# Kernel tuning notes

Measured on AMD Instinct MI355X. Metric: run time of the kernel, lower is better.

The kernel has to match this reference:

```python
import jax, jax.numpy as jnp
import numpy as np

N = 4096      # number of nodes (len(batch_node))
K = 8         # number of adjacency channels
C = 256       # in_channels == out_channels
E = 131072    # number of edges (avg degree 32)


def setup_inputs() -> dict:
    key = jax.random.key(0)
    k1, k2, k3 = jax.random.split(key, 3)
    h = jax.random.normal(k1, (C, N), dtype=jnp.float32)
    X = jax.random.normal(k2, (E, K), dtype=jnp.float32)
    # sample unique (src, dst) pairs so the scatter-set has no duplicate writes
    rng = np.random.default_rng(0)
    flat = rng.choice(N * N, size=E, replace=False)
    edge_index = jnp.asarray(np.stack([flat // N, flat % N]).astype(np.int32))
    batch_node = jnp.zeros((N,), dtype=jnp.float32)
    # glorot uniform: stdv = sqrt(6 / (in + out))
    stdv = np.sqrt(6.0 / (C + C)).astype(np.float32)
    weight = jax.random.uniform(k3, (K, C, C), dtype=jnp.float32,
                                minval=-stdv, maxval=stdv)
    bias = jnp.zeros((C,), dtype=jnp.float32)
    return {"h": h, "X": X, "edge_index": edge_index,
            "batch_node": batch_node, "weight": weight, "bias": bias}


def reference(h, X, edge_index, batch_node, weight, bias):
    Kk = weight.shape[0]
    Nn = batch_node.shape[0]
    # scatter edge features into K dense [N, N] adjacency tensors
    resx = jnp.zeros((Kk, Nn, Nn), dtype=h.dtype)
    resx = resx.at[:, edge_index[0], edge_index[1]].set(X.T)
    # res[k] = h @ resx[k] : [K, C, N]
    res = jnp.einsum('cn,knm->kcm', h, resx)
    # sum_k weight[k] @ res[k] : [C, N]  (in_channels == out_channels)
    out = jnp.einsum('kio,kon->in', weight, res)
    # (res.T + bias).T == res + bias[:, None]
    return out + bias[:, None]
```

## Files before the change

### kernel.cpp

```cpp
#include <hip/hip_runtime.h>

constexpr int NN = 4096;
constexpr int KC = 8;
constexpr int CC = 256;
constexpr int NE = 131072;
constexpr int KK = KC * CC;
constexpr int CAP = 96;

typedef short bf16x8 __attribute__((ext_vector_type(8)));
typedef float f32x4 __attribute__((ext_vector_type(4)));

__device__ inline unsigned short f2bf(float f) {
    union { float f; unsigned int u; } v; v.f = f;
    unsigned int u = v.u;
    u += 0x7fffu + ((u >> 16) & 1u);
    return (unsigned short)(u >> 16);
}
__device__ inline float bf2f(unsigned short u) {
    union { unsigned int i; float f; } w; w.i = ((unsigned int)u) << 16; return w.f;
}

__global__ __launch_bounds__(256) void k_mega(
    const float* __restrict__ h, const float* __restrict__ w,
    const int* __restrict__ edge_src, const int* __restrict__ edge_dst,
    unsigned short* __restrict__ ht, unsigned short* __restrict__ A,
    int* __restrict__ cursor, int2* __restrict__ bins) {
    __shared__ float tile[32][33];
    int b = blockIdx.x;
    int t = threadIdx.x;
    if (b < 512) {
        int e = b * 256 + t;
        int d = edge_dst[e];
        int slot = atomicAdd(&cursor[d], 1);
        if (slot < CAP) bins[d * CAP + slot] = make_int2(e, edge_src[e]);
    } else if (b < 1536) {
        int tt = b - 512;
        int n0 = (tt >> 3) * 32, c0 = (tt & 7) * 32;
        int tx = t & 31, ty = t >> 5;
#pragma unroll
        for (int j = 0; j < 32; j += 8)
            tile[ty + j][tx] = h[(size_t)(c0 + ty + j) * NN + n0 + tx];
        __syncthreads();
#pragma unroll
        for (int j = 0; j < 32; j += 8)
            ht[(size_t)(n0 + ty + j) * CC + c0 + tx] = f2bf(tile[tx][ty + j]);
    } else {
        int g = (b - 1536) * 256 + t;
        int idx = g * 4;
        int o = idx & 255, k = (idx >> 8) & 7, i = idx >> 11;
        float4 wv = *reinterpret_cast<const float4*>(w + ((k << 16) | (i << 8) | o));
        ushort4 av;
        av.x = f2bf(wv.x); av.y = f2bf(wv.y); av.z = f2bf(wv.z); av.w = f2bf(wv.w);
        *reinterpret_cast<ushort4*>(A + idx) = av;
    }
}

__device__ inline void agg_accum(f32x4 acc[KC], float4 v, float4 xa, float4 xb) {
    f32x4 vv = {v.x, v.y, v.z, v.w};
    acc[0] += xa.x * vv; acc[1] += xa.y * vv;
    acc[2] += xa.z * vv; acc[3] += xa.w * vv;
    acc[4] += xb.x * vv; acc[5] += xb.y * vv;
    acc[6] += xb.z * vv; acc[7] += xb.w * vv;
}

__global__ __launch_bounds__(256) void k_agg(
    const int* __restrict__ cursor, const int2* __restrict__ bins,
    const float* __restrict__ X, const unsigned short* __restrict__ ht,
    unsigned short* __restrict__ agg) {
    __shared__ f32x4 part[2][KC][64];
    const int wid  = __builtin_amdgcn_readfirstlane(threadIdx.x >> 6);
    const int lane = threadIdx.x & 63;
    const int m    = wid >> 1;
    const int half = wid & 1;
    const int n = blockIdx.x * 2 + m;
    int cnt = cursor[n];
    cnt = cnt > CAP ? CAP : cnt;
    const int h0 = (cnt + 1) >> 1;
    const int ps = n * CAP + (half ? h0 : 0);
    const int pe = n * CAP + (half ? cnt : h0);
    const float4* X4 = reinterpret_cast<const float4*>(X);

    f32x4 acc[KC] = {};

    int p = ps;
    for (; p + 8 <= pe; p += 8) {
        int2 q[8];
        ushort4 u[8];
#pragma unroll
        for (int j = 0; j < 8; ++j) q[j] = bins[p + j];
#pragma unroll
        for (int j = 0; j < 8; ++j)
            u[j] = *(const ushort4*)(ht + (size_t)q[j].y * CC + 4 * lane);
#pragma unroll
        for (int j = 0; j < 8; ++j) {
            float4 v = {bf2f(u[j].x), bf2f(u[j].y), bf2f(u[j].z), bf2f(u[j].w)};
            agg_accum(acc, v, X4[q[j].x * 2], X4[q[j].x * 2 + 1]);
        }
    }
    for (; p < pe; ++p) {
        int2 q = bins[p];
        ushort4 u = *(const ushort4*)(ht + (size_t)q.y * CC + 4 * lane);
        float4 v = {bf2f(u.x), bf2f(u.y), bf2f(u.z), bf2f(u.w)};
        agg_accum(acc, v, X4[q.x * 2], X4[q.x * 2 + 1]);
    }

    if (half == 1) {
#pragma unroll
        for (int k = 0; k < KC; ++k) part[m][k][lane] = acc[k];
    }
    __syncthreads();
    if (half == 0) {
        unsigned short* op = agg + (size_t)n * KK + 4 * lane;
#pragma unroll
        for (int k = 0; k < KC; ++k) {
            f32x4 s = acc[k] + part[m][k][lane];
            ushort4 w;
            w.x = f2bf(s[0]); w.y = f2bf(s[1]);
            w.z = f2bf(s[2]); w.w = f2bf(s[3]);
            *reinterpret_cast<ushort4*>(op + k * CC) = w;
        }
    }
}

__global__ __launch_bounds__(256) void k_gemm_mfma(
    const unsigned short* __restrict__ A, const unsigned short* __restrict__ B,
    const float* __restrict__ bias, float* __restrict__ out) {
    constexpr int BM = 64, BN = 32, BK = 64;
    constexpr int NT = KK / BK;
    __shared__ unsigned short As[2][BM][BK];
    __shared__ unsigned short Bs[2][BN][BK];
    const int tid  = threadIdx.x;
    const int wid  = tid >> 6;
    const int lane = tid & 63;

    const int raw = blockIdx.x;
    const int swz = (raw & 7) * 64 + (raw >> 3);
    const int i0 = (swz & 3) * BM;
    const int n0 = (swz >> 2) * BN;

    const int wm = (wid & 1) * 32;
    const int wn = (wid >> 1) * 16;

    const int lrow = lane >> 3;
    const int csrc = ((lane & 7) ^ lrow) * 8;

    f32x4 acc[2] = {};

#define STAGE(T, BUF)                                                              \
    do {                                                                           \
        int kc0_ = (T) * BK;                                                       \
        _Pragma("unroll")                                                          \
        for (int q = 0; q < 2; ++q) {                                              \
            int seg = wid + q * 4;                                                 \
            int row = seg * 8 + lrow;                                              \
            __builtin_amdgcn_global_load_lds(                                      \
                (const __attribute__((address_space(1))) void*)(                   \
                    A + (size_t)(i0 + row) * KK + kc0_ + csrc),                    \
                (__attribute__((address_space(3))) void*)(                         \
                    (char*)&As[BUF][0][0] + seg * 1024), 16, 0, 0);                \
        }                                                                          \
        {                                                                          \
            int row = wid * 8 + lrow;                                              \
            __builtin_amdgcn_global_load_lds(                                      \
                (const __attribute__((address_space(1))) void*)(                   \
                    B + (size_t)(n0 + row) * KK + kc0_ + csrc),                    \
                (__attribute__((address_space(3))) void*)(                         \
                    (char*)&Bs[BUF][0][0] + wid * 1024), 16, 0, 0);                \
        }                                                                          \
    } while (0)

    STAGE(0, 0);

    const int rA = wm + (lane & 15);
    const int rB = wn + (lane & 15);
    const int sw = lane & 7;
    const int chb = lane >> 4;

    for (int t = 0; t < NT; ++t) {
        int b = t & 1;
        if (t + 1 < NT) {
            STAGE(t + 1, b ^ 1);
            asm volatile("s_waitcnt vmcnt(3)" ::: "memory");
        } else {
            asm volatile("s_waitcnt vmcnt(0)" ::: "memory");
        }
        __builtin_amdgcn_s_barrier();
        asm volatile("" ::: "memory");

        const char* Ab = (const char*)&As[b][0][0];
        const char* Bb = (const char*)&Bs[b][0][0];
#pragma unroll
        for (int ks = 0; ks < BK; ks += 32) {
            const int ch = (ks >> 3) + chb;
            bf16x8 a0 = *(const bf16x8*)(Ab + rA * 128 + ((ch ^ sw) << 4));
            bf16x8 a1 = *(const bf16x8*)(Ab + (rA + 16) * 128 + ((ch ^ sw) << 4));
            bf16x8 b0 = *(const bf16x8*)(Bb + rB * 128 + ((ch ^ sw) << 4));
            acc[0] = __builtin_amdgcn_mfma_f32_16x16x32_bf16(a0, b0, acc[0], 0, 0, 0);
            acc[1] = __builtin_amdgcn_mfma_f32_16x16x32_bf16(a1, b0, acc[1], 0, 0, 0);
        }
        asm volatile("" ::: "memory");
        __builtin_amdgcn_s_barrier();
    }
#undef STAGE

    const int lr = (lane >> 4) * 4;
    const int lc = lane & 15;
#pragma unroll
    for (int mi = 0; mi < 2; ++mi) {
#pragma unroll
        for (int r = 0; r < 4; ++r) {
            int i = i0 + wm + mi * 16 + lr + r;
            out[(size_t)i * NN + n0 + wn + lc] = acc[mi][r] + bias[i];
        }
    }
}

extern "C" void kernel_launch(void* const* d_in, const int* in_sizes, int n_in,
                              void* d_out, int out_size, void* d_ws, size_t ws_size,
                              hipStream_t stream) {
    const float* h      = (const float*)d_in[0];
    const float* X      = (const float*)d_in[1];
    const int* edge_idx = (const int*)d_in[2];
    const float* weight = (const float*)d_in[4];
    const float* bias   = (const float*)d_in[5];
    float* out = (float*)d_out;

    const int* edge_src = edge_idx;
    const int* edge_dst = edge_idx + NE;

    char* ws = (char*)d_ws;
    unsigned short* ht   = (unsigned short*)(ws);
    unsigned short* Abf  = (unsigned short*)(ws + (2 << 20));
    unsigned short* agg  = (unsigned short*)(ws + (4 << 20));
    size_t meta = (size_t)(20 << 20);
    int* cursor = (int*)(ws + meta);
    int2* bins  = (int2*)(ws + meta + 65536);

    hipMemsetAsync(cursor, 0, NN * sizeof(int), stream);
    k_mega<<<2048, 256, 0, stream>>>(h, weight, edge_src, edge_dst, ht, Abf,
                                     cursor, bins);
    k_agg<<<NN / 2, 256, 0, stream>>>(cursor, bins, X, ht, agg);
    k_gemm_mfma<<<512, 256, 0, stream>>>(Abf, agg, bias, out);
}
```

Measured before the change: 54.01 us.

## Pre-bin bf16 edge features with sources and software-pipeline the aggregation gather

The binning pass now stores each edge's source index in one array and its 8 edge features, converted to packed bf16, in a parallel array. The aggregation kernel then reads X contiguously per node instead of gathering it by edge id. Each wave now handles a whole node, with no half-split or LDS reduction, and the gather loop is double-buffered over batches of 8 edges so loads overlap the FMAs. This rounds X to bf16 before accumulation, which adds precision error, and the extra buffering raises register pressure.

```diff
diff --git a/kernel.cpp b/kernel.cpp
--- a/kernel.cpp
+++ b/kernel.cpp
@@ -19,12 +19,20 @@
 __device__ inline float bf2f(unsigned short u) {
     union { unsigned int i; float f; } w; w.i = ((unsigned int)u) << 16; return w.f;
 }
+__device__ inline float bf_l(unsigned int w) {
+    union { unsigned int i; float f; } t; t.i = w << 16; return t.f;
+}
+__device__ inline float bf_h(unsigned int w) {
+    union { unsigned int i; float f; } t; t.i = w & 0xffff0000u; return t.f;
+}
 
 __global__ __launch_bounds__(256) void k_mega(
     const float* __restrict__ h, const float* __restrict__ w,
+    const float* __restrict__ X,
     const int* __restrict__ edge_src, const int* __restrict__ edge_dst,
     unsigned short* __restrict__ ht, unsigned short* __restrict__ A,
-    int* __restrict__ cursor, int2* __restrict__ bins) {
+    int* __restrict__ cursor, int* __restrict__ binsS,
+    uint4* __restrict__ binsX) {
     __shared__ float tile[32][33];
     int b = blockIdx.x;
     int t = threadIdx.x;
@@ -32,7 +40,18 @@
         int e = b * 256 + t;
         int d = edge_dst[e];
         int slot = atomicAdd(&cursor[d], 1);
-        if (slot < CAP) bins[d * CAP + slot] = make_int2(e, edge_src[e]);
+        if (slot < CAP) {
+            int p = d * CAP + slot;
+            binsS[p] = edge_src[e];
+            const float4* xp = reinterpret_cast<const float4*>(X + (size_t)e * 8);
+            float4 xa = xp[0], xb = xp[1];
+            uint4 xw;
+            xw.x = (unsigned)f2bf(xa.x) | ((unsigned)f2bf(xa.y) << 16);
+            xw.y = (unsigned)f2bf(xa.z) | ((unsigned)f2bf(xa.w) << 16);
+            xw.z = (unsigned)f2bf(xb.x) | ((unsigned)f2bf(xb.y) << 16);
+            xw.w = (unsigned)f2bf(xb.z) | ((unsigned)f2bf(xb.w) << 16);
+            binsX[p] = xw;
+        }
     } else if (b < 1536) {
         int tt = b - 512;
         int n0 = (tt >> 3) * 32, c0 = (tt & 7) * 32;
@@ -55,70 +74,90 @@
     }
 }
 
-__device__ inline void agg_accum(f32x4 acc[KC], float4 v, float4 xa, float4 xb) {
-    f32x4 vv = {v.x, v.y, v.z, v.w};
-    acc[0] += xa.x * vv; acc[1] += xa.y * vv;
-    acc[2] += xa.z * vv; acc[3] += xa.w * vv;
-    acc[4] += xb.x * vv; acc[5] += xb.y * vv;
-    acc[6] += xb.z * vv; acc[7] += xb.w * vv;
+__device__ inline void edge_fma(f32x4 acc[KC], uint2 u, uint4 xw) {
+    f32x4 v = {bf_l(u.x), bf_h(u.x), bf_l(u.y), bf_h(u.y)};
+    acc[0] += bf_l(xw.x) * v;  acc[1] += bf_h(xw.x) * v;
+    acc[2] += bf_l(xw.y) * v;  acc[3] += bf_h(xw.y) * v;
+    acc[4] += bf_l(xw.z) * v;  acc[5] += bf_h(xw.z) * v;
+    acc[6] += bf_l(xw.w) * v;  acc[7] += bf_h(xw.w) * v;
 }
 
 __global__ __launch_bounds__(256) void k_agg(
-    const int* __restrict__ cursor, const int2* __restrict__ bins,
-    const float* __restrict__ X, const unsigned short* __restrict__ ht,
+    const int* __restrict__ cursor, const int* __restrict__ binsS,
+    const uint4* __restrict__ binsX, const unsigned short* __restrict__ ht,
     unsigned short* __restrict__ agg) {
-    __shared__ f32x4 part[2][KC][64];
     const int wid  = __builtin_amdgcn_readfirstlane(threadIdx.x >> 6);
     const int lane = threadIdx.x & 63;
-    const int m    = wid >> 1;
-    const int half = wid & 1;
-    const int n = blockIdx.x * 2 + m;
+    const int n = blockIdx.x * 4 + wid;
     int cnt = cursor[n];
     cnt = cnt > CAP ? CAP : cnt;
-    const int h0 = (cnt + 1) >> 1;
-    const int ps = n * CAP + (half ? h0 : 0);
-    const int pe = n * CAP + (half ? cnt : h0);
-    const float4* X4 = reinterpret_cast<const float4*>(X);
+    const int base = n * CAP;
+    const int ch = 4 * lane;
 
     f32x4 acc[KC] = {};
 
-    int p = ps;
-    for (; p + 8 <= pe; p += 8) {
-        int2 q[8];
-        ushort4 u[8];
-#pragma unroll
-        for (int j = 0; j < 8; ++j) q[j] = bins[p + j];
-#pragma unroll
-        for (int j = 0; j < 8; ++j)
-            u[j] = *(const ushort4*)(ht + (size_t)q[j].y * CC + 4 * lane);
-#pragma unroll
-        for (int j = 0; j < 8; ++j) {
-            float4 v = {bf2f(u[j].x), bf2f(u[j].y), bf2f(u[j].z), bf2f(u[j].w)};
-            agg_accum(acc, v, X4[q[j].x * 2], X4[q[j].x * 2 + 1]);
-        }
-    }
-    for (; p < pe; ++p) {
-        int2 q = bins[p];
-        ushort4 u = *(const ushort4*)(ht + (size_t)q.y * CC + 4 * lane);
-        float4 v = {bf2f(u.x), bf2f(u.y), bf2f(u.z), bf2f(u.w)};
-        agg_accum(acc, v, X4[q.x * 2], X4[q.x * 2 + 1]);
-    }
-
-    if (half == 1) {
-#pragma unroll
-        for (int k = 0; k < KC; ++k) part[m][k][lane] = acc[k];
-    }
-    __syncthreads();
-    if (half == 0) {
-        unsigned short* op = agg + (size_t)n * KK + 4 * lane;
-#pragma unroll
-        for (int k = 0; k < KC; ++k) {
-            f32x4 s = acc[k] + part[m][k][lane];
-            ushort4 w;
-            w.x = f2bf(s[0]); w.y = f2bf(s[1]);
-            w.z = f2bf(s[2]); w.w = f2bf(s[3]);
-            *reinterpret_cast<ushort4*>(op + k * CC) = w;
-        }
+#define LD_S(S_, bi) do {                                                   \
+        const int4* sp_ = (const int4*)(binsS + base + (bi) * 8);           \
+        int4 a_ = sp_[0], b_ = sp_[1];                                      \
+        S_[0]=a_.x; S_[1]=a_.y; S_[2]=a_.z; S_[3]=a_.w;                     \
+        S_[4]=b_.x; S_[5]=b_.y; S_[6]=b_.z; S_[7]=b_.w; } while (0)
+#define LD_X(X_, bi) do {                                                   \
+        _Pragma("unroll")                                                   \
+        for (int j_ = 0; j_ < 8; ++j_) X_[j_] = binsX[base + (bi)*8 + j_];  \
+    } while (0)
+#define GATH(U_, S_) do {                                                   \
+        _Pragma("unroll")                                                   \
+        for (int j_ = 0; j_ < 8; ++j_)                                      \
+            U_[j_] = *(const uint2*)(ht + (size_t)S_[j_] * CC + ch);        \
+    } while (0)
+#define FMA8(U_, X_) do {                                                   \
+        _Pragma("unroll")                                                   \
+        for (int j_ = 0; j_ < 8; ++j_) edge_fma(acc, U_[j_], X_[j_]);       \
+    } while (0)
+
+    const int nb = cnt >> 3;
+    if (nb >= 2) {
+        int  sA[8], sB[8];
+        uint4 xA[8], xB[8];
+        uint2 uA[8], uB[8];
+        int t = 0;
+        if (nb & 1) {
+            LD_S(sA, 0); LD_X(xA, 0); GATH(uA, sA); FMA8(uA, xA);
+            t = 1;
+        }
+        LD_S(sA, t); LD_X(xA, t);
+        LD_S(sB, t + 1); LD_X(xB, t + 1);
+        GATH(uA, sA);
+        for (; t < nb; t += 2) {
+            GATH(uB, sB);
+            FMA8(uA, xA);
+            bool more = (t + 2 < nb);
+            if (more) { LD_S(sA, t + 2); LD_X(xA, t + 2); GATH(uA, sA); }
+            FMA8(uB, xB);
+            if (more) { LD_S(sB, t + 3); LD_X(xB, t + 3); }
+        }
+    } else if (nb == 1) {
+        int s1[8]; uint4 x1[8]; uint2 u1[8];
+        LD_S(s1, 0); LD_X(x1, 0); GATH(u1, s1); FMA8(u1, x1);
+    }
+    for (int p = base + (cnt & ~7); p < base + cnt; ++p) {
+        int src = binsS[p];
+        uint4 xw = binsX[p];
+        uint2 u = *(const uint2*)(ht + (size_t)src * CC + ch);
+        edge_fma(acc, u, xw);
+    }
+#undef LD_S
+#undef LD_X
+#undef GATH
+#undef FMA8
+
+    unsigned short* op = agg + (size_t)n * KK + ch;
+#pragma unroll
+    for (int k = 0; k < KC; ++k) {
+        ushort4 w;
+        w.x = f2bf(acc[k][0]); w.y = f2bf(acc[k][1]);
+        w.z = f2bf(acc[k][2]); w.w = f2bf(acc[k][3]);
+        *reinterpret_cast<ushort4*>(op + k * CC) = w;
     }
 }
 
@@ -233,12 +272,13 @@
     unsigned short* Abf  = (unsigned short*)(ws + (2 << 20));
     unsigned short* agg  = (unsigned short*)(ws + (4 << 20));
     size_t meta = (size_t)(20 << 20);
-    int* cursor = (int*)(ws + meta);
-    int2* bins  = (int2*)(ws + meta + 65536);
+    int*   cursor = (int*)(ws + meta);
+    int*   binsS  = (int*)(ws + meta + (1 << 20));
+    uint4* binsX  = (uint4*)(ws + meta + (4 << 20));
 
     hipMemsetAsync(cursor, 0, NN * sizeof(int), stream);
-    k_mega<<<2048, 256, 0, stream>>>(h, weight, edge_src, edge_dst, ht, Abf,
-                                     cursor, bins);
-    k_agg<<<NN / 2, 256, 0, stream>>>(cursor, bins, X, ht, agg);
+    k_mega<<<2048, 256, 0, stream>>>(h, weight, X, edge_src, edge_dst, ht, Abf,
+                                     cursor, binsS, binsX);
+    k_agg<<<NN / 4, 256, 0, stream>>>(cursor, binsS, binsX, ht, agg);
     k_gemm_mfma<<<512, 256, 0, stream>>>(Abf, agg, bias, out);
 }
```

Result: no change. 54.85 us (+1.6%).

## Fuse edge binning into aggregation kernel with grid-wide spin barrier; drop memset

Applied to the files above, without the earlier changes.

Removes the separate hipMemsetAsync by zeroing cursor and a done counter inside the prep kernel. Edge binning moves from the prep kernel into the first 512 blocks of the aggregation kernel, and every block spins on the global done counter before it aggregates. This cuts one launch and one memset. The spin barrier assumes the first 512 blocks become resident and finish before the waiting blocks fill the device, which is a deadlock risk if they do not.

```diff
diff --git a/kernel.cpp b/kernel.cpp
--- a/kernel.cpp
+++ b/kernel.cpp
@@ -20,22 +20,16 @@
     union { unsigned int i; float f; } w; w.i = ((unsigned int)u) << 16; return w.f;
 }
 
-__global__ __launch_bounds__(256) void k_mega(
+__global__ __launch_bounds__(256) void k_prep(
     const float* __restrict__ h, const float* __restrict__ w,
-    const int* __restrict__ edge_src, const int* __restrict__ edge_dst,
     unsigned short* __restrict__ ht, unsigned short* __restrict__ A,
-    int* __restrict__ cursor, int2* __restrict__ bins) {
-    __shared__ float tile[32][33];
+    int* __restrict__ cursor, int* __restrict__ done) {
     int b = blockIdx.x;
     int t = threadIdx.x;
-    if (b < 512) {
-        int e = b * 256 + t;
-        int d = edge_dst[e];
-        int slot = atomicAdd(&cursor[d], 1);
-        if (slot < CAP) bins[d * CAP + slot] = make_int2(e, edge_src[e]);
-    } else if (b < 1536) {
-        int tt = b - 512;
-        int n0 = (tt >> 3) * 32, c0 = (tt & 7) * 32;
+    if (b < 1024) {
+        __shared__ float tile[32][33];
+        int nb = b >> 3, cb = b & 7;
+        int n0 = nb * 32, c0 = cb * 32;
         int tx = t & 31, ty = t >> 5;
 #pragma unroll
         for (int j = 0; j < 32; j += 8)
@@ -45,7 +39,9 @@
         for (int j = 0; j < 32; j += 8)
             ht[(size_t)(n0 + ty + j) * CC + c0 + tx] = f2bf(tile[tx][ty + j]);
     } else {
-        int g = (b - 1536) * 256 + t;
+        int g = (b - 1024) * 256 + t;
+        if (g < NN) cursor[g] = 0;
+        if (g == NN) *done = 0;
         int idx = g * 4;
         int o = idx & 255, k = (idx >> 8) & 7, i = idx >> 11;
         float4 wv = *reinterpret_cast<const float4*>(w + ((k << 16) | (i << 8) | o));
@@ -63,16 +59,38 @@
     acc[6] += xb.z * vv; acc[7] += xb.w * vv;
 }
 
-__global__ __launch_bounds__(256) void k_agg(
-    const int* __restrict__ cursor, const int2* __restrict__ bins,
+__global__ __launch_bounds__(256) void k_fillagg(
+    const int* __restrict__ edge_src, const int* __restrict__ edge_dst,
+    int* __restrict__ cursor, int2* __restrict__ bins, int* __restrict__ done,
     const float* __restrict__ X, const unsigned short* __restrict__ ht,
     unsigned short* __restrict__ agg) {
     __shared__ f32x4 part[2][KC][64];
-    const int wid  = __builtin_amdgcn_readfirstlane(threadIdx.x >> 6);
-    const int lane = threadIdx.x & 63;
+    const int b = blockIdx.x;
+    const int t = threadIdx.x;
+
+    if (b < 512) {
+        int e = b * 256 + t;
+        int d = edge_dst[e];
+        int slot = atomicAdd(&cursor[d], 1);
+        if (slot < CAP) bins[d * CAP + slot] = make_int2(e, edge_src[e]);
+        __threadfence();
+        __syncthreads();
+        if (t == 0) atomicAdd(done, 1);
+    }
+
+    if (t == 0) {
+        while (__hip_atomic_load(done, __ATOMIC_ACQUIRE,
+                                 __HIP_MEMORY_SCOPE_AGENT) < 512) {
+            __builtin_amdgcn_s_sleep(32);
+        }
+    }
+    __syncthreads();
+
+    const int wid  = __builtin_amdgcn_readfirstlane(t >> 6);
+    const int lane = t & 63;
     const int m    = wid >> 1;
     const int half = wid & 1;
-    const int n = blockIdx.x * 2 + m;
+    const int n = b * 2 + m;
     int cnt = cursor[n];
     cnt = cnt > CAP ? CAP : cnt;
     const int h0 = (cnt + 1) >> 1;
@@ -234,11 +252,11 @@
     unsigned short* agg  = (unsigned short*)(ws + (4 << 20));
     size_t meta = (size_t)(20 << 20);
     int* cursor = (int*)(ws + meta);
+    int* done   = (int*)(ws + meta + 32768);
     int2* bins  = (int2*)(ws + meta + 65536);
 
-    hipMemsetAsync(cursor, 0, NN * sizeof(int), stream);
-    k_mega<<<2048, 256, 0, stream>>>(h, weight, edge_src, edge_dst, ht, Abf,
-                                     cursor, bins);
-    k_agg<<<NN / 2, 256, 0, stream>>>(cursor, bins, X, ht, agg);
+    k_prep<<<1536, 256, 0, stream>>>(h, weight, ht, Abf, cursor, done);
+    k_fillagg<<<NN / 2, 256, 0, stream>>>(edge_src, edge_dst, cursor, bins,
+                                          done, X, ht, agg);
     k_gemm_mfma<<<512, 256, 0, stream>>>(Abf, agg, bias, out);
 }
```

New measurement: 176.8 us. 3.27x slower.
